# Kernel optimization log

Measured on AMD Instinct MI355X. Metric: run time of the kernel, lower is better.

Reference implementation:

```python
import jax, jax.numpy as jnp
import numpy as np

B, N, D = 4, 4096, 1024
HEADS = 4
DH = D // HEADS
FF = 4 * D
EPS = 1e-5


def layer_norm(x, g, b):
    mu = jnp.mean(x, axis=-1, keepdims=True)
    var = jnp.mean(jnp.square(x - mu), axis=-1, keepdims=True)
    return (x - mu) * jax.lax.rsqrt(var + EPS) * g + b


def linear_attn(q, k, v):
    # q,k,v: [b, h, n, dh]; non-causal kernelized linear attention
    scale = DH ** -0.25
    q = jax.nn.softmax(q * scale, axis=-1)   # feature map over head dim
    k = jax.nn.softmax(k * scale, axis=-2)   # normalized over sequence
    context = jnp.einsum('bhnd,bhne->bhde', k, v)  # [b,h,dh,dh]
    return jnp.einsum('bhnd,bhde->bhne', q, context)


def setup_inputs() -> dict:
    key = jax.random.key(0)
    ks = jax.random.split(key, 16)
    s = lambda fan_in: 1.0 / np.sqrt(fan_in)
    inp = {
        'x': jax.random.normal(ks[0], (B, N, D), jnp.float32),
        # attention block (PreNorm)
        'ln1_g': jnp.ones((D,), jnp.float32),
        'ln1_b': jnp.zeros((D,), jnp.float32),
        'wq': jax.random.normal(ks[1], (D, D), jnp.float32) * s(D),
        'wk': jax.random.normal(ks[2], (D, D), jnp.float32) * s(D),
        'wv': jax.random.normal(ks[3], (D, D), jnp.float32) * s(D),
        'wo': jax.random.normal(ks[4], (D, D), jnp.float32) * s(D),
        'bo': jnp.zeros((D,), jnp.float32),
        # feedforward block (PreNorm)
        'ln2_g': jnp.ones((D,), jnp.float32),
        'ln2_b': jnp.zeros((D,), jnp.float32),
        'w_ff1': jax.random.normal(ks[5], (D, FF), jnp.float32) * s(D),
        'b_ff1': jnp.zeros((FF,), jnp.float32),
        'w_ff2': jax.random.normal(ks[6], (FF, D), jnp.float32) * s(FF),
        'b_ff2': jnp.zeros((D,), jnp.float32),
        # trailing dense
        'w_d': jax.random.normal(ks[7], (D, D), jnp.float32) * s(D),
        'b_d': jnp.zeros((D,), jnp.float32),
    }
    return inp


def reference(x, ln1_g, ln1_b, wq, wk, wv, wo, bo, ln2_g, ln2_b,
              w_ff1, b_ff1, w_ff2, b_ff2, w_d, b_d):
    b, n, d = x.shape
    # --- PreNorm linear self-attention + residual ---
    h = layer_norm(x, ln1_g, ln1_b)
    q = (h @ wq).reshape(b, n, HEADS, DH).transpose(0, 2, 1, 3)
    k = (h @ wk).reshape(b, n, HEADS, DH).transpose(0, 2, 1, 3)
    v = (h @ wv).reshape(b, n, HEADS, DH).transpose(0, 2, 1, 3)
    attn = linear_attn(q, k, v)                      # [b,h,n,dh]
    attn = attn.transpose(0, 2, 1, 3).reshape(b, n, d)
    x = x + attn @ wo + bo
    # --- PreNorm FFN (GELU, mult=4) + residual ---
    h = layer_norm(x, ln2_g, ln2_b)
    x = x + jax.nn.gelu(h @ w_ff1 + b_ff1) @ w_ff2 + b_ff2
    # --- trailing dense projection ---
    return x @ w_d + b_d
```

## Files before the change

### kernel.cpp

```cpp
#include <hip/hip_runtime.h>
#include <hip/hip_bf16.h>


typedef __hip_bfloat16 bf16;
typedef __attribute__((ext_vector_type(8))) short short8;
typedef __attribute__((ext_vector_type(4))) float floatx4;

__device__ __forceinline__ float b2f(bf16 x) { return __bfloat162float(x); }
__device__ __forceinline__ bf16 f2b(float x) { return __float2bfloat16(x); }
__device__ __forceinline__ float s2f(short s) {
  unsigned int u = ((unsigned int)(unsigned short)s) << 16;
  return __uint_as_float(u);
}
__device__ __forceinline__ short f2s(float f) {
  bf16 h = __float2bfloat16(f);
  return *reinterpret_cast<short*>(&h);
}
__device__ __forceinline__ float gelu_f(float x) {
  float u = 0.7978845608028654f * (x + 0.044715f * x * x * x);
  return 0.5f * x * (1.0f + tanhf(u));
}

template <int TRANSC, int AFP32, int CFP32, int ATOM, int RESF32 = 0>
__global__ __launch_bounds__(256) void gemm_bt(
    const void* __restrict__ Aop, const bf16* __restrict__ BT, void* Cv,
    int K, int lda, int ldb, int ldc, int zshift,
    long saA, long shA, long saB, long shB, long saC, long shC,
    const float* __restrict__ bias, const bf16* res, int act,
    const float2* stats, const float* __restrict__ gamma,
    const float* __restrict__ beta)
{
  int z = blockIdx.z;
  int zb = z >> zshift, zh = z & ((1 << zshift) - 1);
  long offA = (long)zb * saA + (long)zh * shA;
  long offC = (long)zb * saC + (long)zh * shC;
  const float* Af = (const float*)Aop + offA;
  const bf16*  Ab = (const bf16*)Aop + offA;
  BT += (long)zb * saB + (long)zh * shB;
  bf16*  C  = (bf16*)Cv + offC;
  float* Cf = (float*)Cv + offC;
  const bf16*  resb = res ? res + offC : nullptr;
  const float* resf = res ? (const float*)res + offC : nullptr;
  if (stats) stats += offA / lda;

  __shared__ bf16 smem[TRANSC ? 128 * 136 : 16384];
  bf16* As = smem;
  bf16* Bs = smem + 8192;

  const int t = threadIdx.x;
  const int w = t >> 6, l = t & 63;
  const int m0 = blockIdx.y * 128, n0 = blockIdx.x * 128;
  const int wm = (w >> 1) * 64, wn = (w & 1) * 64;
  const int lr = l & 15, lq = l >> 4;

  floatx4 acc[4][4] = {};

  const int sr = t >> 2;
  const int sc = (t & 3) * 8;
  const int stO = sr * 32 + (((t & 3) ^ ((sr >> 1) & 3))) * 8;
  const int rowA0 = m0 + sr, rowA1 = m0 + 64 + sr;
  const long o0 = (long)rowA0 * lda + sc;
  const long o1 = (long)rowA1 * lda + sc;

  const bf16* Bp0 = BT + (long)(n0 + sr) * ldb + sc;
  const bf16* Bp1 = BT + (long)(n0 + 64 + sr) * ldb + sc;

  float2 st0, st1;
  if (stats) { st0 = stats[rowA0]; st1 = stats[rowA1]; }

  auto LOADSET = [&](int k0, short8& ra0, short8& ra1, short8& rb0, short8& rb1) {
    if constexpr (AFP32) {
      float4 a00 = *(const float4*)(Af + o0 + k0);
      float4 a01 = *(const float4*)(Af + o0 + k0 + 4);
      float4 a10 = *(const float4*)(Af + o1 + k0);
      float4 a11 = *(const float4*)(Af + o1 + k0 + 4);
      float v0[8] = {a00.x, a00.y, a00.z, a00.w, a01.x, a01.y, a01.z, a01.w};
      float v1[8] = {a10.x, a10.y, a10.z, a10.w, a11.x, a11.y, a11.z, a11.w};
      if (stats) {
        float4 g0 = *(const float4*)(gamma + k0 + sc);
        float4 g1 = *(const float4*)(gamma + k0 + sc + 4);
        float4 e0 = *(const float4*)(beta + k0 + sc);
        float4 e1 = *(const float4*)(beta + k0 + sc + 4);
        float gv[8] = {g0.x, g0.y, g0.z, g0.w, g1.x, g1.y, g1.z, g1.w};
        float ev[8] = {e0.x, e0.y, e0.z, e0.w, e1.x, e1.y, e1.z, e1.w};
#pragma unroll
        for (int i = 0; i < 8; i++) {
          v0[i] = (v0[i] - st0.x) * st0.y * gv[i] + ev[i];
          v1[i] = (v1[i] - st1.x) * st1.y * gv[i] + ev[i];
        }
      }
#pragma unroll
      for (int i = 0; i < 8; i++) { ra0[i] = f2s(v0[i]); ra1[i] = f2s(v1[i]); }
    } else {
      ra0 = *(const short8*)(Ab + o0 + k0);
      ra1 = *(const short8*)(Ab + o1 + k0);
      if (stats) {
        float4 g0 = *(const float4*)(gamma + k0 + sc);
        float4 g1 = *(const float4*)(gamma + k0 + sc + 4);
        float4 e0 = *(const float4*)(beta + k0 + sc);
        float4 e1 = *(const float4*)(beta + k0 + sc + 4);
        float gv[8] = {g0.x, g0.y, g0.z, g0.w, g1.x, g1.y, g1.z, g1.w};
        float ev[8] = {e0.x, e0.y, e0.z, e0.w, e1.x, e1.y, e1.z, e1.w};
#pragma unroll
        for (int i = 0; i < 8; i++) {
          ra0[i] = f2s((s2f(ra0[i]) - st0.x) * st0.y * gv[i] + ev[i]);
          ra1[i] = f2s((s2f(ra1[i]) - st1.x) * st1.y * gv[i] + ev[i]);
        }
      }
    }
    short8 b0 = *(const short8*)(Bp0 + k0);
    short8 b1 = *(const short8*)(Bp1 + k0);
    rb0 = b0; rb1 = b1;
  };

  auto STORESET = [&](int p, short8 ra0, short8 ra1, short8 rb0, short8 rb1) {
    *(short8*)&As[p * 4096 + stO]        = ra0;
    *(short8*)&As[p * 4096 + 2048 + stO] = ra1;
    *(short8*)&Bs[p * 4096 + stO]        = rb0;
    *(short8*)&Bs[p * 4096 + 2048 + stO] = rb1;
  };

  auto COMPUTE = [&](int p) {
    short8 af[4], bfr[4];
#pragma unroll
    for (int i = 0; i < 4; i++) {
      int Ra = wm + i * 16 + lr;
      int Rb = wn + i * 16 + lr;
      af[i]  = *(const short8*)&As[p * 4096 + Ra * 32 + (lq ^ ((Ra >> 1) & 3)) * 8];
      bfr[i] = *(const short8*)&Bs[p * 4096 + Rb * 32 + (lq ^ ((Rb >> 1) & 3)) * 8];
    }
#pragma unroll
    for (int i = 0; i < 4; i++)
#pragma unroll
      for (int j = 0; j < 4; j++)
        acc[i][j] = __builtin_amdgcn_mfma_f32_16x16x32_bf16(af[i], bfr[j], acc[i][j], 0, 0, 0);
  };

  short8 pa0, pa1, pb0, pb1, qa0, qa1, qb0, qb1;
  LOADSET(0,  pa0, pa1, pb0, pb1);
  LOADSET(32, qa0, qa1, qb0, qb1);
  STORESET(0, pa0, pa1, pb0, pb1);
  __syncthreads();
  const int nI = K >> 5;
  for (int it = 0; it < nI; it += 2) {
    if (it + 2 < nI) LOADSET((it + 2) * 32, pa0, pa1, pb0, pb1);
    COMPUTE(0);
    STORESET(1, qa0, qa1, qb0, qb1);
    __syncthreads();
    if (it + 3 < nI) LOADSET((it + 3) * 32, qa0, qa1, qb0, qb1);
    COMPUTE(1);
    if (it + 2 < nI) STORESET(0, pa0, pa1, pb0, pb1);
    __syncthreads();
  }

  if constexpr (TRANSC) {
    bf16* TC = smem;
#pragma unroll
    for (int i = 0; i < 4; i++) {
      int rloc = wm + i * 16 + lq * 4;
#pragma unroll
      for (int j = 0; j < 4; j++) {
        int cloc = wn + j * 16 + lr;
#pragma unroll
        for (int r = 0; r < 4; r++)
          TC[cloc * 136 + rloc + r] = f2b(acc[i][j][r]);
      }
    }
    __syncthreads();
    long base = (long)n0 * ldc + m0;
#pragma unroll
    for (int p = 0; p < 8; p++) {
      int er = (t >> 4) + p * 16;
      int mc = (t & 15) * 8;
      *(short8*)(C + base + (long)er * ldc + mc) = *(const short8*)&TC[er * 136 + mc];
    }
    return;
  }

#pragma unroll
  for (int i = 0; i < 4; i++) {
    int row0 = m0 + wm + i * 16 + lq * 4;
#pragma unroll
    for (int j = 0; j < 4; j++) {
      int col = n0 + wn + j * 16 + lr;
      if constexpr (ATOM) {
#pragma unroll
        for (int r = 0; r < 4; r++) {
          long idx = (long)(row0 + r) * ldc + col;
          atomicAdd(&Cf[idx], acc[i][j][r]);
        }
      } else {
        float bv = bias ? bias[col] : 0.0f;
#pragma unroll
        for (int r = 0; r < 4; r++) {
          float v = acc[i][j][r] + bv;
          long idx = (long)(row0 + r) * ldc + col;
          if (res) {
            if constexpr (RESF32) v += resf[idx]; else v += b2f(resb[idx]);
          }
          if (act) v = gelu_f(v);
          if constexpr (CFP32) Cf[idx] = v; else C[idx] = f2b(v);
        }
      }
    }
  }
}

__global__ void transpose_f2b(const float* __restrict__ src, bf16* __restrict__ dst,
                              int lsrc, int ldst)
{
  __shared__ bf16 tile[32][33];
  int tx = threadIdx.x, ty = threadIdx.y;
  int c0 = blockIdx.x * 32, r0 = blockIdx.y * 32;
#pragma unroll
  for (int j = 0; j < 4; j++)
    tile[ty + j * 8][tx] = f2b(src[(long)(r0 + ty + j * 8) * lsrc + c0 + tx]);
  __syncthreads();
#pragma unroll
  for (int j = 0; j < 4; j++)
    dst[(long)(c0 + ty + j * 8) * ldst + r0 + tx] = tile[tx][ty + j * 8];
}

__global__ __launch_bounds__(128) void copy_cols(const bf16* __restrict__ s,
                                                 bf16* __restrict__ d)
{
  int r = blockIdx.x, c = threadIdx.x * 8;
  *(short8*)(d + (long)r * 5120 + 4096 + c) = *(const short8*)(s + (long)r * 1024 + c);
}

__global__ __launch_bounds__(256) void ln_stats_f32(
    const float* __restrict__ x, float2* __restrict__ stats)
{
  int row = blockIdx.x, t = threadIdx.x;
  const float* xr = x + (long)row * 1024;
  float4 a = *(const float4*)(xr + t * 4);
  float s = a.x + a.y + a.z + a.w;
  float q = a.x * a.x + a.y * a.y + a.z * a.z + a.w * a.w;
  for (int o = 32; o > 0; o >>= 1) { s += __shfl_down(s, o); q += __shfl_down(q, o); }
  __shared__ float sm[8];
  if ((t & 63) == 0) { sm[t >> 6] = s; sm[4 + (t >> 6)] = q; }
  __syncthreads();
  if (t == 0) {
    s = sm[0] + sm[1] + sm[2] + sm[3];
    q = sm[4] + sm[5] + sm[6] + sm[7];
    float mean = s * (1.0f / 1024.0f);
    float var  = q * (1.0f / 1024.0f) - mean * mean;
    stats[row] = make_float2(mean, rsqrtf(var + 1e-5f));
  }
}

__global__ __launch_bounds__(256) void ln_apply(
    const float* __restrict__ x, const float2* __restrict__ stats,
    const float* __restrict__ g, const float* __restrict__ b,
    bf16* __restrict__ out)
{
  long i = ((long)blockIdx.x * 256 + threadIdx.x) * 8;
  int row = (int)(i >> 10), col = (int)(i & 1023);
  float2 st = stats[row];
  float4 a0 = *(const float4*)(x + i);
  float4 a1 = *(const float4*)(x + i + 4);
  float4 g0 = *(const float4*)(g + col);
  float4 g1 = *(const float4*)(g + col + 4);
  float4 b0 = *(const float4*)(b + col);
  float4 b1 = *(const float4*)(b + col + 4);
  float av[8] = {a0.x, a0.y, a0.z, a0.w, a1.x, a1.y, a1.z, a1.w};
  float gv[8] = {g0.x, g0.y, g0.z, g0.w, g1.x, g1.y, g1.z, g1.w};
  float bv[8] = {b0.x, b0.y, b0.z, b0.w, b1.x, b1.y, b1.z, b1.w};
  short8 o;
#pragma unroll
  for (int j = 0; j < 8; j++)
    o[j] = f2s((av[j] - st.x) * st.y * gv[j] + bv[j]);
  *(short8*)(out + i) = o;
}

__global__ __launch_bounds__(256) void ln_stats_b16(
    const bf16* __restrict__ x, float2* __restrict__ stats)
{
  int row = blockIdx.x, t = threadIdx.x;
  const bf16* xr = x + (long)row * 1024;
  float v[4];
#pragma unroll
  for (int i = 0; i < 4; i++) v[i] = b2f(xr[t * 4 + i]);
  float s = v[0] + v[1] + v[2] + v[3];
  float q = v[0] * v[0] + v[1] * v[1] + v[2] * v[2] + v[3] * v[3];
  for (int o = 32; o > 0; o >>= 1) { s += __shfl_down(s, o); q += __shfl_down(q, o); }
  __shared__ float sm[8];
  if ((t & 63) == 0) { sm[t >> 6] = s; sm[4 + (t >> 6)] = q; }
  __syncthreads();
  if (t == 0) {
    s = sm[0] + sm[1] + sm[2] + sm[3];
    q = sm[4] + sm[5] + sm[6] + sm[7];
    float mean = s * (1.0f / 1024.0f);
    float var  = q * (1.0f / 1024.0f) - mean * mean;
    stats[row] = make_float2(mean, rsqrtf(var + 1e-5f));
  }
}

__global__ __launch_bounds__(256) void qsoftmax256(bf16* __restrict__ q)
{
  long idx = (long)blockIdx.x * 256 + threadIdx.x;
  int t = threadIdx.x;
  float v = expf(0.25f * b2f(q[idx]));
  float s = v;
  for (int o = 32; o > 0; o >>= 1) s += __shfl_down(s, o);
  __shared__ float sm[4];
  if ((t & 63) == 0) sm[t >> 6] = s;
  __syncthreads();
  float tot = sm[0] + sm[1] + sm[2] + sm[3];
  q[idx] = f2b(v / tot);
}

__global__ __launch_bounds__(256) void ksoftmaxKV(bf16* __restrict__ kv)
{
  int b = blockIdx.x >> 8, e = blockIdx.x & 255;
  long base = ((long)b * 512 + e) * 4096;
  int t = threadIdx.x;
  float loc[16];
  float s = 0.0f;
#pragma unroll
  for (int i = 0; i < 16; i++) {
    loc[i] = expf(0.25f * b2f(kv[base + t + i * 256]));
    s += loc[i];
  }
  for (int o = 32; o > 0; o >>= 1) s += __shfl_down(s, o);
  __shared__ float sm[4];
  if ((t & 63) == 0) sm[t >> 6] = s;
  __syncthreads();
  float inv = 1.0f / (sm[0] + sm[1] + sm[2] + sm[3]);
#pragma unroll
  for (int i = 0; i < 16; i++)
    kv[base + t + i * 256] = f2b(loc[i] * inv);
}

__global__ __launch_bounds__(256) void reduce_ctx(
    const bf16* __restrict__ G, bf16* __restrict__ CTX)
{
  long i = (long)blockIdx.x * 256 + threadIdx.x;
  float s = 0.0f;
#pragma unroll
  for (int kc = 0; kc < 8; kc++) s += b2f(G[kc * 262144 + i]);
  CTX[i] = f2b(s);
}

__global__ __launch_bounds__(256) void out_bias(
    const float* __restrict__ b2, const bf16* __restrict__ wdt, int ld,
    const float* __restrict__ bd, float* __restrict__ OB)
{
  int n = blockIdx.x, t = threadIdx.x;
  const bf16* wr = wdt + (long)n * ld;
  float s = 0.0f;
#pragma unroll
  for (int i = 0; i < 4; i++) {
    int k = t * 4 + i;
    s += b2[k] * b2f(wr[k]);
  }
  for (int o = 32; o > 0; o >>= 1) s += __shfl_down(s, o);
  __shared__ float sm[4];
  if ((t & 63) == 0) sm[t >> 6] = s;
  __syncthreads();
  if (t == 0) OB[n] = sm[0] + sm[1] + sm[2] + sm[3] + bd[n];
}

__global__ __launch_bounds__(256) void bias_bcast(
    const float* __restrict__ b, float* __restrict__ out)
{
  long i = ((long)blockIdx.x * 256 + threadIdx.x) * 4;
  *(float4*)(out + i) = *(const float4*)(b + (int)(i & 1023));
}

extern "C" void kernel_launch(void* const* d_in, const int* in_sizes, int n_in,
                              void* d_out, int out_size, void* d_ws, size_t ws_size,
                              hipStream_t stream) {
  const float* x    = (const float*)d_in[0];
  const float* ln1g = (const float*)d_in[1];
  const float* ln1b = (const float*)d_in[2];
  const float* wq   = (const float*)d_in[3];
  const float* wk   = (const float*)d_in[4];
  const float* wv   = (const float*)d_in[5];
  const float* wo   = (const float*)d_in[6];
  const float* bo   = (const float*)d_in[7];
  const float* ln2g = (const float*)d_in[8];
  const float* ln2b = (const float*)d_in[9];
  const float* wff1 = (const float*)d_in[10];
  const float* bff1 = (const float*)d_in[11];
  const float* wff2 = (const float*)d_in[12];
  const float* bff2 = (const float*)d_in[13];
  const float* wd   = (const float*)d_in[14];
  const float* bd   = (const float*)d_in[15];

  bf16* xln = (bf16*)d_out;
  bf16* x2  = (bf16*)d_out + (size_t)16384 * 1024;
  float* outf = (float*)d_out;

  char* wsp = (char*)d_ws;
  size_t off = 0;
  auto alloc = [&](size_t bytes) -> void* {
    void* p = wsp + off; off += (bytes + 255) & ~(size_t)255; return p;
  };
  bf16*   S1  = (bf16*)alloc((size_t)8 * 1024 * 1024);
  bf16*   S2  = (bf16*)alloc((size_t)10 * 1024 * 1024);
  bf16*   G   = (bf16*)alloc((size_t)10 * 1024 * 1024);
  bf16*   CTX = (bf16*)alloc((size_t)4 * 256 * 256 * 2);
  bf16*   W1  = (bf16*)alloc((size_t)1024 * 256 * 2);
  float2* st1 = (float2*)alloc((size_t)16384 * 8);
  float2* st2 = (float2*)alloc((size_t)16384 * 8);
  bf16*   KV  = S1;
  bf16*   W1kv = G + (size_t)9 * 512 * 1024;
  bf16*   WB  = S2;
  float*  OB  = (float*)CTX;

  const long SA  = (long)4096 * 1024;
  const long PKV = (long)512 * 4096;
  dim3 tb(32, 8);
  const bf16* nb = nullptr;

  ln_stats_f32<<<16384, 256, 0, stream>>>(x, st1);
  ln_apply<<<8192, 256, 0, stream>>>(x, st1, ln1g, ln1b, xln);

  for (int h = 0; h < 4; h++) {
    transpose_f2b<<<dim3(8, 32), tb, 0, stream>>>(wk + h * 256, W1kv, 1024, 1024);
    transpose_f2b<<<dim3(8, 32), tb, 0, stream>>>(wv + h * 256, W1kv + 256 * 1024, 1024, 1024);
    gemm_bt<1, 0, 0, 0><<<dim3(4, 32, 4), 256, 0, stream>>>(xln, W1kv, KV,
        1024, 1024, 1024, 4096, 2, 0, SA, 0, 0, 0, PKV,
        nullptr, nb, 0, nullptr, nullptr, nullptr);
    ksoftmaxKV<<<1024, 256, 0, stream>>>(KV);

    gemm_bt<0, 0, 0, 0><<<dim3(2, 2, 32), 256, 0, stream>>>(KV + (long)256 * 4096, KV, G,
        512, 4096, 4096, 256, 3, PKV, 512, PKV, 512, 65536, 262144,
        nullptr, nb, 0, nullptr, nullptr, nullptr);
    reduce_ctx<<<1024, 256, 0, stream>>>(G, CTX);

    transpose_f2b<<<dim3(8, 32), tb, 0, stream>>>(wq + h * 256, W1, 1024, 1024);
    gemm_bt<0, 0, 0, 0><<<dim3(2, 32, 4), 256, 0, stream>>>(xln, W1, S1,
        1024, 1024, 1024, 256, 2, 0, SA, 0, 0, 0, (long)4096 * 256,
        nullptr, nb, 0, nullptr, nullptr, nullptr);
    qsoftmax256<<<16384, 256, 0, stream>>>(S1);

    gemm_bt<0, 0, 0, 0><<<dim3(2, 32, 4), 256, 0, stream>>>(S1, CTX, S2,
        256, 256, 256, 256, 2, 0, (long)4096 * 256, 0, 65536, 0, (long)4096 * 256,
        nullptr, nb, 0, nullptr, nullptr, nullptr);

    transpose_f2b<<<dim3(32, 8), tb, 0, stream>>>(wo + (size_t)h * 256 * 1024, W1, 1024, 256);
    if (h == 0)
      gemm_bt<0, 0, 0, 0, 1><<<dim3(8, 128, 1), 256, 0, stream>>>(S2, W1, x2,
          256, 256, 256, 1024, 2, 0, 0, 0, 0, 0, 0,
          bo, (const bf16*)x, 0, nullptr, nullptr, nullptr);
    else
      gemm_bt<0, 0, 0, 0, 0><<<dim3(8, 128, 1), 256, 0, stream>>>(S2, W1, x2,
          256, 256, 256, 1024, 2, 0, 0, 0, 0, 0, 0,
          nullptr, x2, 0, nullptr, nullptr, nullptr);
  }

  ln_stats_b16<<<16384, 256, 0, stream>>>(x2, st2);
  transpose_f2b<<<dim3(128, 32), tb, 0, stream>>>(wff1, S1, 4096, 1024);
  transpose_f2b<<<dim3(32, 32), tb, 0, stream>>>(wd, WB + 4096, 1024, 5120);
  gemm_bt<1, 1, 0, 0><<<dim3(8, 32, 1), 256, 0, stream>>>(wff2, WB + 4096, WB,
      1024, 1024, 5120, 5120, 0, 0, 0, 0, 0, 0, 0,
      nullptr, nb, 0, nullptr, nullptr, nullptr);
  out_bias<<<1024, 256, 0, stream>>>(bff2, WB + 4096, 5120, bd, OB);

  for (int R = 0; R < 16; R++) {
    const bf16* xr = x2 + (size_t)R * 1024 * 1024;
    copy_cols<<<1024, 128, 0, stream>>>(xr, G);
    gemm_bt<0, 0, 0, 0><<<dim3(32, 8, 1), 256, 0, stream>>>(xr, S1, G,
        1024, 1024, 1024, 5120, 2, 0, 0, 0, 0, 0, 0,
        bff1, nb, 1, st2 + R * 1024, ln2g, ln2b);
    bias_bcast<<<1024, 256, 0, stream>>>(OB, outf + (size_t)R * 1024 * 1024);
    gemm_bt<0, 0, 1, 1><<<dim3(8, 8, 8), 256, 0, stream>>>(G, WB,
        outf + (size_t)R * 1024 * 1024,
        640, 5120, 5120, 1024, 3, 0, 640, 0, 640, 0, 0,
        nullptr, nb, 0, nullptr, nullptr, nullptr);
  }
}
```

Baseline: 2.253 ms.

## Fold per-head context into output projection and run full-width Q GEMMs

Restructures attention: the per-head loop now only computes K/V projections and contexts (with more K-splits in the context GEMM), then multiplies the context by Wo once to form combined per-head weights. Q projection, softmax, and the fused context*Wo projection with bias and residual are done as full-width GEMMs in two batch halves instead of four per-head passes of narrow GEMMs. This cuts the launch count and replaces the small K=256 GEMMs with larger, better-shaped ones. The FF2 split-K is also reduced from 8 to 4, which changes atomic traffic and per-block work.

After: 1.970 ms. 12.5% less time.

```diff
diff --git a/kernel.cpp b/kernel.cpp
--- a/kernel.cpp
+++ b/kernel.cpp
@@ -333,13 +333,13 @@
 }
 
 __global__ __launch_bounds__(256) void reduce_ctx(
-    const bf16* __restrict__ G, bf16* __restrict__ CTX)
+    const bf16* __restrict__ G, bf16* __restrict__ dst)
 {
   long i = (long)blockIdx.x * 256 + threadIdx.x;
   float s = 0.0f;
 #pragma unroll
-  for (int kc = 0; kc < 8; kc++) s += b2f(G[kc * 262144 + i]);
-  CTX[i] = f2b(s);
+  for (int kc = 0; kc < 16; kc++) s += b2f(G[kc * 262144 + i]);
+  dst[(i >> 16) * 262144 + (i & 65535)] = f2b(s);
 }
 
 __global__ __launch_bounds__(256) void out_bias(
@@ -404,10 +404,15 @@
   bf16*   W1  = (bf16*)alloc((size_t)1024 * 256 * 2);
   float2* st1 = (float2*)alloc((size_t)16384 * 8);
   float2* st2 = (float2*)alloc((size_t)16384 * 8);
-  bf16*   KV  = S1;
+  bf16*   KV   = S1;
   bf16*   W1kv = G + (size_t)9 * 512 * 1024;
-  bf16*   WB  = S2;
-  float*  OB  = (float*)CTX;
+  bf16*   CTXT = S2 + (size_t)4 * 1024 * 1024;
+  bf16*   woT  = G + (size_t)4 * 1024 * 1024;
+  bf16*   CWT  = G;
+  bf16*   wqT  = CTXT;
+  bf16*   QB   = S1;
+  bf16*   WB   = S2;
+  float*  OB   = (float*)CTX;
 
   const long SA  = (long)4096 * 1024;
   const long PKV = (long)512 * 4096;
@@ -425,30 +430,29 @@
         nullptr, nb, 0, nullptr, nullptr, nullptr);
     ksoftmaxKV<<<1024, 256, 0, stream>>>(KV);
 
-    gemm_bt<0, 0, 0, 0><<<dim3(2, 2, 32), 256, 0, stream>>>(KV + (long)256 * 4096, KV, G,
-        512, 4096, 4096, 256, 3, PKV, 512, PKV, 512, 65536, 262144,
+    gemm_bt<0, 0, 0, 0><<<dim3(2, 2, 64), 256, 0, stream>>>(KV, KV + (long)256 * 4096, G,
+        256, 4096, 4096, 256, 4, PKV, 256, PKV, 256, 65536, 262144,
         nullptr, nb, 0, nullptr, nullptr, nullptr);
-    reduce_ctx<<<1024, 256, 0, stream>>>(G, CTX);
-
-    transpose_f2b<<<dim3(8, 32), tb, 0, stream>>>(wq + h * 256, W1, 1024, 1024);
-    gemm_bt<0, 0, 0, 0><<<dim3(2, 32, 4), 256, 0, stream>>>(xln, W1, S1,
-        1024, 1024, 1024, 256, 2, 0, SA, 0, 0, 0, (long)4096 * 256,
+    reduce_ctx<<<1024, 256, 0, stream>>>(G, CTXT + h * 65536);
+  }
+
+  transpose_f2b<<<dim3(32, 32), tb, 0, stream>>>(wo, woT, 1024, 1024);
+  gemm_bt<0, 0, 0, 0><<<dim3(2, 8, 16), 256, 0, stream>>>(woT, CTXT, CWT,
+      256, 1024, 256, 1024, 2, 0, 256, 262144, 65536, 1048576, 256,
+      nullptr, nb, 0, nullptr, nullptr, nullptr);
+  transpose_f2b<<<dim3(32, 32), tb, 0, stream>>>(wq, wqT, 1024, 1024);
+
+  for (int p = 0; p < 2; p++) {
+    gemm_bt<0, 0, 0, 0><<<dim3(8, 64, 1), 256, 0, stream>>>(
+        xln + (size_t)p * 8192 * 1024, wqT, QB,
+        1024, 1024, 1024, 1024, 0, 0, 0, 0, 0, 0, 0,
         nullptr, nb, 0, nullptr, nullptr, nullptr);
-    qsoftmax256<<<16384, 256, 0, stream>>>(S1);
-
-    gemm_bt<0, 0, 0, 0><<<dim3(2, 32, 4), 256, 0, stream>>>(S1, CTX, S2,
-        256, 256, 256, 256, 2, 0, (long)4096 * 256, 0, 65536, 0, (long)4096 * 256,
-        nullptr, nb, 0, nullptr, nullptr, nullptr);
-
-    transpose_f2b<<<dim3(32, 8), tb, 0, stream>>>(wo + (size_t)h * 256 * 1024, W1, 1024, 256);
-    if (h == 0)
-      gemm_bt<0, 0, 0, 0, 1><<<dim3(8, 128, 1), 256, 0, stream>>>(S2, W1, x2,
-          256, 256, 256, 1024, 2, 0, 0, 0, 0, 0, 0,
-          bo, (const bf16*)x, 0, nullptr, nullptr, nullptr);
-    else
-      gemm_bt<0, 0, 0, 0, 0><<<dim3(8, 128, 1), 256, 0, stream>>>(S2, W1, x2,
-          256, 256, 256, 1024, 2, 0, 0, 0, 0, 0, 0,
-          nullptr, x2, 0, nullptr, nullptr, nullptr);
+    qsoftmax256<<<32768, 256, 0, stream>>>(QB);
+    gemm_bt<0, 0, 0, 0, 1><<<dim3(8, 32, 2), 256, 0, stream>>>(
+        QB, CWT + (size_t)p * 2 * 1048576, x2 + (size_t)p * 8192 * 1024,
+        1024, 1024, 1024, 1024, 1, 0, SA, 0, 1048576, 0, SA,
+        bo, (const bf16*)(x + (size_t)p * 8192 * 1024), 0,
+        nullptr, nullptr, nullptr);
   }
 
   ln_stats_b16<<<16384, 256, 0, stream>>>(x2, st2);
@@ -466,9 +470,9 @@
         1024, 1024, 1024, 5120, 2, 0, 0, 0, 0, 0, 0,
         bff1, nb, 1, st2 + R * 1024, ln2g, ln2b);
     bias_bcast<<<1024, 256, 0, stream>>>(OB, outf + (size_t)R * 1024 * 1024);
-    gemm_bt<0, 0, 1, 1><<<dim3(8, 8, 8), 256, 0, stream>>>(G, WB,
+    gemm_bt<0, 0, 1, 1><<<dim3(8, 8, 4), 256, 0, stream>>>(G, WB,
         outf + (size_t)R * 1024 * 1024,
-        640, 5120, 5120, 1024, 3, 0, 640, 0, 640, 0, 0,
+        1280, 5120, 5120, 1024, 2, 0, 1280, 0, 1280, 0, 0,
         nullptr, nb, 0, nullptr, nullptr, nullptr);
   }
 }
```
